# Kernel optimization log

Measured on AMD Instinct MI355X. Metric: run time of the kernel, lower is better.

Reference implementation:

```python
import jax, jax.numpy as jnp
import numpy as np

N_HEADS = 16
ROPE_THETA = 10000.0


def _rope_tables(seq_len, head_dim, dtype=jnp.float32):
    half = head_dim // 2
    inv_freq = 1.0 / (ROPE_THETA ** (jnp.arange(0, half, dtype=jnp.float32) / half))
    t = jnp.arange(seq_len, dtype=jnp.float32)
    freqs = jnp.outer(t, inv_freq)  # (S, half)
    return jnp.cos(freqs).astype(dtype), jnp.sin(freqs).astype(dtype)


def _apply_rope(x, cos, sin):
    # x: (B, H, S, hd); cos/sin: (S, hd//2)
    half = x.shape[-1] // 2
    x1, x2 = x[..., :half], x[..., half:]
    c = cos[None, None, :, :]
    s = sin[None, None, :, :]
    return jnp.concatenate([x1 * c - x2 * s, x1 * s + x2 * c], axis=-1)


def setup_inputs() -> dict:
    key = jax.random.key(0)
    k1, k2, k3 = jax.random.split(key, 3)
    B, S, D = 4, 2048, 2048
    hd = D // N_HEADS
    x = jax.random.normal(k1, (B, S, D), dtype=jnp.float32)
    cos, sin = _rope_tables(S, hd)
    w_qkv = jax.random.normal(k2, (D, 3 * D), dtype=jnp.float32) * (D ** -0.5)
    w_out = jax.random.normal(k3, (D, D), dtype=jnp.float32) * (D ** -0.5)
    return {"x": x, "cos": cos, "sin": sin, "w_qkv": w_qkv, "w_out": w_out}


def reference(x, cos, sin, w_qkv, w_out):
    B, S, D = x.shape
    H = N_HEADS
    hd = D // H
    qkv = x @ w_qkv  # (B, S, 3D)
    qkv = qkv.reshape(B, S, 3, H, hd).transpose(2, 0, 3, 1, 4)  # (3, B, H, S, hd)
    q, k, v = qkv[0], qkv[1], qkv[2]
    q = _apply_rope(q, cos, sin)
    k = _apply_rope(k, cos, sin)
    scale = 1.0 / jnp.sqrt(jnp.asarray(hd, dtype=x.dtype))
    scores = jnp.einsum('bhqd,bhkd->bhqk', q, k) * scale  # (B, H, S, S)
    causal = jnp.tril(jnp.ones((S, S), dtype=bool))
    scores = jnp.where(causal[None, None, :, :], scores, jnp.asarray(-1e30, dtype=scores.dtype))
    p = jax.nn.softmax(scores, axis=-1)
    out = jnp.einsum('bhqk,bhkd->bhqd', p, v)  # (B, H, S, hd)
    out = out.transpose(0, 2, 1, 3).reshape(B, S, D)
    return out @ w_out
```

## Files before the change

kernel.cpp:

```cpp
#include <hip/hip_runtime.h>
#include <stdint.h>

typedef __bf16  bf16x8  __attribute__((ext_vector_type(8)));
typedef float   floatx4 __attribute__((ext_vector_type(4)));

typedef __attribute__((address_space(1))) void gvoid_t;
typedef __attribute__((address_space(3))) void svoid_t;

__device__ __forceinline__ void gld16(ushort* lds, const ushort* g) {
  __builtin_amdgcn_global_load_lds((gvoid_t*)g, (svoid_t*)lds, 16, 0, 0);
}

__device__ __forceinline__ ushort f2bf(float f) {
  union { float f; unsigned u; } v; v.f = f;
  unsigned u = v.u;
  return (ushort)((u + 0x7fffu + ((u >> 16) & 1u)) >> 16);
}
__device__ __forceinline__ float bf2f(ushort h) {
  union { unsigned u; float f; } v; v.u = ((unsigned)h) << 16; return v.f;
}

__device__ __forceinline__ float qmax16(float v) {
  v = fmaxf(v, __shfl_xor(v, 1));
  v = fmaxf(v, __shfl_xor(v, 2));
  v = fmaxf(v, __shfl_xor(v, 4));
  v = fmaxf(v, __shfl_xor(v, 8));
  return v;
}
__device__ __forceinline__ float qsum16(float v) {
  v += __shfl_xor(v, 1);
  v += __shfl_xor(v, 2);
  v += __shfl_xor(v, 4);
  v += __shfl_xor(v, 8);
  return v;
}

__global__ __launch_bounds__(256) void cvt_f32_bf16(
    const float* __restrict__ in, ushort* __restrict__ out) {
  int i = blockIdx.x * 256 + threadIdx.x;
  float4 a = ((const float4*)in)[i];
  ushort4 o;
  o.x = f2bf(a.x); o.y = f2bf(a.y); o.z = f2bf(a.z); o.w = f2bf(a.w);
  ((ushort4*)out)[i] = o;
}

__global__ __launch_bounds__(256) void transpose_cvt(
    const float* __restrict__ in, ushort* __restrict__ out, int R, int C) {
  __shared__ ushort tile[64][65];
  const int r0 = blockIdx.y * 64, c0 = blockIdx.x * 64;
  const int t = threadIdx.x;
#pragma unroll
  for (int rep = 0; rep < 16; rep++) {
    int idx = rep * 256 + t;
    int r = idx >> 6, c = idx & 63;
    tile[r][c] = f2bf(in[(size_t)(r0 + r) * C + c0 + c]);
  }
  __syncthreads();
#pragma unroll
  for (int rep = 0; rep < 16; rep++) {
    int idx = rep * 256 + t;
    int r = idx >> 6, c = idx & 63;
    out[(size_t)(c0 + r) * R + r0 + c] = tile[c][r];
  }
}

template <int EPI>
__global__ __launch_bounds__(256) void gemm128(
    const ushort* __restrict__ A, const ushort* __restrict__ Bt,
    float* __restrict__ Cf,
    ushort* __restrict__ C0, ushort* __restrict__ C1, ushort* __restrict__ C2,
    int M, int N, int K) {
  __shared__ __align__(16) ushort As[128 * 64];
  __shared__ __align__(16) ushort Bs[128 * 64];
  const int t = threadIdx.x;
  const int lane = t & 63;
  const int w = t >> 6;
  const int l15 = lane & 15;
  const int quad = lane >> 4;
  const int m0 = blockIdx.y * 128;
  const int n0 = blockIdx.x * 128;
  const int wm = (w >> 1) * 64;
  const int wn = (w & 1) * 64;

  floatx4 acc[4][4];
  const floatx4 zero = {0.f, 0.f, 0.f, 0.f};
#pragma unroll
  for (int i = 0; i < 4; i++)
#pragma unroll
    for (int j = 0; j < 4; j++) acc[i][j] = zero;

  for (int kb = 0; kb < K; kb += 64) {
    __syncthreads();
#pragma unroll
    for (int it = 0; it < 4; it++) {
      int o = (w * 4 + it) * 64 + lane;
      int row = o >> 3;
      int c = (o & 7) ^ (row & 7);
      gld16(&As[(w * 4 + it) * 512], A + (size_t)(m0 + row) * K + kb + c * 8);
      gld16(&Bs[(w * 4 + it) * 512], Bt + (size_t)(n0 + row) * K + kb + c * 8);
    }
    __syncthreads();
#pragma unroll
    for (int kk = 0; kk < 2; kk++) {
      bf16x8 af[4], bf[4];
#pragma unroll
      for (int i = 0; i < 4; i++) {
        int row = wm + i * 16 + l15;
        int c = (kk * 4 + quad) ^ (row & 7);
        af[i] = *(const bf16x8*)&As[row * 64 + c * 8];
      }
#pragma unroll
      for (int j = 0; j < 4; j++) {
        int row = wn + j * 16 + l15;
        int c = (kk * 4 + quad) ^ (row & 7);
        bf[j] = *(const bf16x8*)&Bs[row * 64 + c * 8];
      }
#pragma unroll
      for (int i = 0; i < 4; i++)
#pragma unroll
        for (int j = 0; j < 4; j++)
          acc[i][j] = __builtin_amdgcn_mfma_f32_16x16x32_bf16(af[i], bf[j],
                                                              acc[i][j], 0, 0, 0);
    }
  }

  if (EPI == 0) {
#pragma unroll
    for (int i = 0; i < 4; i++)
#pragma unroll
      for (int j = 0; j < 4; j++)
#pragma unroll
        for (int r = 0; r < 4; r++) {
          int m = m0 + wm + i * 16 + quad * 4 + r;
          int n = n0 + wn + j * 16 + l15;
          Cf[(size_t)m * N + n] = acc[i][j][r];
        }
  } else {
    const int qkvsel = n0 >> 11;
    const int h = (n0 >> 7) & 15;
#pragma unroll
    for (int i = 0; i < 4; i++)
#pragma unroll
      for (int j = 0; j < 4; j++) {
        int d = wn + j * 16 + l15;
        if (qkvsel < 2) {
          ushort* dst = (qkvsel == 0) ? C0 : C1;
#pragma unroll
          for (int r = 0; r < 4; r++) {
            int m = m0 + wm + i * 16 + quad * 4 + r;
            int b = m >> 11, s = m & 2047;
            dst[((size_t)(b * 16 + h) * 2048 + s) * 128 + d] = f2bf(acc[i][j][r]);
          }
        } else {
          int m = m0 + wm + i * 16 + quad * 4;
          int b = m >> 11, s = m & 2047;
          ushort4 pk;
          pk.x = f2bf(acc[i][j][0]);
          pk.y = f2bf(acc[i][j][1]);
          pk.z = f2bf(acc[i][j][2]);
          pk.w = f2bf(acc[i][j][3]);
          *(ushort4*)&C2[((size_t)(b * 16 + h) * 128 + d) * 2048 + s] = pk;
        }
      }
  }
}

__global__ __launch_bounds__(256) void rope_kernel(
    ushort* __restrict__ Q, ushort* __restrict__ Kb,
    const float* __restrict__ cosT, const float* __restrict__ sinT) {
  unsigned gid = blockIdx.x * 256u + threadIdx.x;
  int d = gid & 63;
  int s = (gid >> 6) & 2047;
  int bh = (gid >> 17) & 63;
  ushort* buf = (gid >> 23) ? Kb : Q;
  size_t base = ((size_t)bh * 2048 + s) * 128;
  float x1 = bf2f(buf[base + d]);
  float x2 = bf2f(buf[base + d + 64]);
  float c = cosT[s * 64 + d];
  float sn = sinT[s * 64 + d];
  buf[base + d] = f2bf(x1 * c - x2 * sn);
  buf[base + d + 64] = f2bf(x1 * sn + x2 * c);
}

__global__ __launch_bounds__(256, 4) void attn_kernel(
    const ushort* __restrict__ Q, const ushort* __restrict__ Kb,
    const ushort* __restrict__ VT, ushort* __restrict__ O) {
  __shared__ __align__(16) ushort Ks[64 * 128];
  __shared__ __align__(16) ushort Vs[128 * 64];
  __shared__ __align__(16) ushort Ps[64 * 64];
  const int t = threadIdx.x, lane = t & 63, w = t >> 6;
  const int l15 = lane & 15, quad = lane >> 4;
  const int bid = blockIdx.x;
  const int tq = 31 - (bid >> 6);
  const int bh = bid & 63;
  const int q0 = tq * 64 + w * 16;
  const size_t hbase = (size_t)bh * 2048 * 128;
  const float NEGINF = -__builtin_inff();

  bf16x8 aq[4];
#pragma unroll
  for (int kb = 0; kb < 4; kb++)
    aq[kb] = *(const bf16x8*)&Q[hbase + (size_t)(q0 + l15) * 128 +
                                kb * 32 + quad * 8];

  float m2[4], lsum[4];
  floatx4 oacc[8];
  const floatx4 zero = {0.f, 0.f, 0.f, 0.f};
#pragma unroll
  for (int r = 0; r < 4; r++) { m2[r] = NEGINF; lsum[r] = 0.f; }
#pragma unroll
  for (int dj = 0; dj < 8; dj++) oacc[dj] = zero;

  const float sl2e = 0.08838834764831845f * 1.4426950408889634f;
  const int ntk = tq + 1;

  for (int tk = 0; tk < ntk; tk++) {
    __syncthreads();
#pragma unroll
    for (int it = 0; it < 4; it++) {
      int o = (w * 4 + it) * 64 + lane;
      {
        int row = o >> 4;
        int c = (o & 15) ^ (row & 15);
        gld16(&Ks[(w * 4 + it) * 512],
              Kb + hbase + (size_t)(tk * 64 + row) * 128 + c * 8);
      }
      {
        int row = o >> 3;
        int c = (o & 7) ^ (row & 7);
        gld16(&Vs[(w * 4 + it) * 512],
              VT + hbase + (size_t)row * 2048 + tk * 64 + c * 8);
      }
    }
    __syncthreads();

    floatx4 sacc[4];
#pragma unroll
    for (int j = 0; j < 4; j++) sacc[j] = zero;
#pragma unroll
    for (int kb = 0; kb < 4; kb++) {
#pragma unroll
      for (int j = 0; j < 4; j++) {
        int row = j * 16 + l15;
        int c = (kb * 4 + quad) ^ (row & 15);
        bf16x8 bk = *(const bf16x8*)&Ks[row * 128 + c * 8];
        sacc[j] = __builtin_amdgcn_mfma_f32_16x16x32_bf16(aq[kb], bk, sacc[j],
                                                          0, 0, 0);
      }
    }

    const bool need_mask = (tk == tq);
#pragma unroll
    for (int j = 0; j < 4; j++)
#pragma unroll
      for (int r = 0; r < 4; r++) {
        float v = sacc[j][r] * sl2e;
        if (need_mask) {
          int col = tk * 64 + j * 16 + l15;
          int row = q0 + quad * 4 + r;
          if (col > row) v = NEGINF;
        }
        sacc[j][r] = v;
      }
#pragma unroll
    for (int r = 0; r < 4; r++) {
      float mx = fmaxf(fmaxf(sacc[0][r], sacc[1][r]),
                       fmaxf(sacc[2][r], sacc[3][r]));
      mx = qmax16(mx);
      float mnew = fmaxf(m2[r], mx);
      float alpha = __builtin_exp2f(m2[r] - mnew);
      m2[r] = mnew;
      float rs = 0.f;
#pragma unroll
      for (int j = 0; j < 4; j++) {
        float p = __builtin_exp2f(sacc[j][r] - mnew);
        sacc[j][r] = p;
        rs += p;
      }
      rs = qsum16(rs);
      lsum[r] = lsum[r] * alpha + rs;
#pragma unroll
      for (int dj = 0; dj < 8; dj++) oacc[dj][r] *= alpha;
    }

#pragma unroll
    for (int j = 0; j < 4; j++)
#pragma unroll
      for (int r = 0; r < 4; r++) {
        int prow = w * 16 + quad * 4 + r;
        int col = j * 16 + l15;
        int scol = (((col >> 3) ^ (prow & 7)) << 3) | (col & 7);
        Ps[prow * 64 + scol] = f2bf(sacc[j][r]);
      }

    bf16x8 ap[2];
#pragma unroll
    for (int kk = 0; kk < 2; kk++) {
      int row = w * 16 + l15;
      int c = (kk * 4 + quad) ^ (row & 7);
      ap[kk] = *(const bf16x8*)&Ps[row * 64 + c * 8];
    }
#pragma unroll
    for (int kk = 0; kk < 2; kk++)
#pragma unroll
      for (int dj = 0; dj < 8; dj++) {
        int rowd = dj * 16 + l15;
        int c = (kk * 4 + quad) ^ (rowd & 7);
        bf16x8 bv = *(const bf16x8*)&Vs[rowd * 64 + c * 8];
        oacc[dj] = __builtin_amdgcn_mfma_f32_16x16x32_bf16(ap[kk], bv, oacc[dj],
                                                           0, 0, 0);
      }
  }

  const int b = bh >> 4, h = bh & 15;
  float rinv[4];
#pragma unroll
  for (int r = 0; r < 4; r++) rinv[r] = 1.0f / lsum[r];
#pragma unroll
  for (int dj = 0; dj < 8; dj++) {
    int d = dj * 16 + l15;
#pragma unroll
    for (int r = 0; r < 4; r++) {
      int q = q0 + quad * 4 + r;
      O[((size_t)(b * 2048 + q)) * 2048 + h * 128 + d] =
          f2bf(oacc[dj][r] * rinv[r]);
    }
  }
}

extern "C" void kernel_launch(void* const* d_in, const int* in_sizes, int n_in,
                              void* d_out, int out_size, void* d_ws, size_t ws_size,
                              hipStream_t stream) {
  const float* x    = (const float*)d_in[0];
  const float* cosT = (const float*)d_in[1];
  const float* sinT = (const float*)d_in[2];
  const float* wqkv = (const float*)d_in[3];
  const float* wout = (const float*)d_in[4];
  float* out = (float*)d_out;
  char* ws = (char*)d_ws;

  ushort* xbf   = (ushort*)d_out;
  ushort* wqkvT = (ushort*)(ws);
  ushort* Ob    = (ushort*)(ws);
  ushort* woutT = (ushort*)(ws + 33554432);
  ushort* Qb    = (ushort*)(ws + 41943040);
  ushort* Kbuf  = (ushort*)(ws + 75497472);
  ushort* VTb   = (ushort*)(ws + 109051904);

  cvt_f32_bf16<<<16384, 256, 0, stream>>>(x, xbf);
  transpose_cvt<<<dim3(96, 32), 256, 0, stream>>>(wqkv, wqkvT, 2048, 6144);
  transpose_cvt<<<dim3(32, 32), 256, 0, stream>>>(wout, woutT, 2048, 2048);
  gemm128<1><<<dim3(48, 64), 256, 0, stream>>>(xbf, wqkvT, nullptr,
                                               Qb, Kbuf, VTb, 8192, 6144, 2048);
  rope_kernel<<<65536, 256, 0, stream>>>(Qb, Kbuf, cosT, sinT);
  attn_kernel<<<2048, 256, 0, stream>>>(Qb, Kbuf, VTb, Ob);
  gemm128<0><<<dim3(16, 64), 256, 0, stream>>>(Ob, woutT, out,
                                               nullptr, nullptr, nullptr,
                                               8192, 2048, 2048);
}
```

Baseline: 730.0 us.

## Transpose attention MFMAs so each lane owns one query row

The QK^T and PV MFMA operand order is swapped, so the score and output accumulators are transposed and each lane holds a single query row. Softmax max and sum then reduce within the lane plus two cross-quad shuffles instead of 16-lane shuffle trees, and the per-row state collapses to scalars. The softmax scale and log2e factor are folded into Q during RoPE. P is written to LDS with packed bf16 stores, output is written with vectorized 4-element stores, and the rescale of the O accumulator is skipped when no row's max changed. Folding the scale into Q before bf16 rounding changes numerics slightly.

```diff
diff --git a/kernel.cpp b/kernel.cpp
--- a/kernel.cpp
+++ b/kernel.cpp
@@ -1,4 +1,5 @@
 #include <hip/hip_runtime.h>
+#include <hip/hip_bf16.h>
 #include <stdint.h>
 
 typedef __bf16  bf16x8  __attribute__((ext_vector_type(8)));
@@ -19,20 +20,9 @@
 __device__ __forceinline__ float bf2f(ushort h) {
   union { unsigned u; float f; } v; v.u = ((unsigned)h) << 16; return v.f;
 }
-
-__device__ __forceinline__ float qmax16(float v) {
-  v = fmaxf(v, __shfl_xor(v, 1));
-  v = fmaxf(v, __shfl_xor(v, 2));
-  v = fmaxf(v, __shfl_xor(v, 4));
-  v = fmaxf(v, __shfl_xor(v, 8));
-  return v;
-}
-__device__ __forceinline__ float qsum16(float v) {
-  v += __shfl_xor(v, 1);
-  v += __shfl_xor(v, 2);
-  v += __shfl_xor(v, 4);
-  v += __shfl_xor(v, 8);
-  return v;
+__device__ __forceinline__ unsigned pk2bf(float a, float b) {
+  __hip_bfloat162 h = __float22bfloat162_rn(make_float2(a, b));
+  union { __hip_bfloat162 h; unsigned u; } v; v.h = h; return v.u;
 }
 
 __global__ __launch_bounds__(256) void cvt_f32_bf16(
@@ -172,14 +162,17 @@
   int d = gid & 63;
   int s = (gid >> 6) & 2047;
   int bh = (gid >> 17) & 63;
-  ushort* buf = (gid >> 23) ? Kb : Q;
+  const bool isK = (gid >> 23) != 0;
+  ushort* buf = isK ? Kb : Q;
+  const float sc = isK ? 1.0f
+                       : 0.08838834764831845f * 1.4426950408889634f;
   size_t base = ((size_t)bh * 2048 + s) * 128;
   float x1 = bf2f(buf[base + d]);
   float x2 = bf2f(buf[base + d + 64]);
   float c = cosT[s * 64 + d];
   float sn = sinT[s * 64 + d];
-  buf[base + d] = f2bf(x1 * c - x2 * sn);
-  buf[base + d + 64] = f2bf(x1 * sn + x2 * c);
+  buf[base + d] = f2bf((x1 * c - x2 * sn) * sc);
+  buf[base + d + 64] = f2bf((x1 * sn + x2 * c) * sc);
 }
 
 __global__ __launch_bounds__(256, 4) void attn_kernel(
@@ -194,24 +187,21 @@
   const int tq = 31 - (bid >> 6);
   const int bh = bid & 63;
   const int q0 = tq * 64 + w * 16;
+  const int qrow = q0 + l15;
   const size_t hbase = (size_t)bh * 2048 * 128;
   const float NEGINF = -__builtin_inff();
 
   bf16x8 aq[4];
 #pragma unroll
   for (int kb = 0; kb < 4; kb++)
-    aq[kb] = *(const bf16x8*)&Q[hbase + (size_t)(q0 + l15) * 128 +
-                                kb * 32 + quad * 8];
-
-  float m2[4], lsum[4];
+    aq[kb] = *(const bf16x8*)&Q[hbase + (size_t)qrow * 128 + kb * 32 + quad * 8];
+
+  float m2 = NEGINF, lsum = 0.f;
   floatx4 oacc[8];
   const floatx4 zero = {0.f, 0.f, 0.f, 0.f};
 #pragma unroll
-  for (int r = 0; r < 4; r++) { m2[r] = NEGINF; lsum[r] = 0.f; }
-#pragma unroll
   for (int dj = 0; dj < 8; dj++) oacc[dj] = zero;
 
-  const float sl2e = 0.08838834764831845f * 1.4426950408889634f;
   const int ntk = tq + 1;
 
   for (int tk = 0; tk < ntk; tk++) {
@@ -243,62 +233,65 @@
       for (int j = 0; j < 4; j++) {
         int row = j * 16 + l15;
         int c = (kb * 4 + quad) ^ (row & 15);
-        bf16x8 bk = *(const bf16x8*)&Ks[row * 128 + c * 8];
-        sacc[j] = __builtin_amdgcn_mfma_f32_16x16x32_bf16(aq[kb], bk, sacc[j],
+        bf16x8 kf = *(const bf16x8*)&Ks[row * 128 + c * 8];
+        sacc[j] = __builtin_amdgcn_mfma_f32_16x16x32_bf16(kf, aq[kb], sacc[j],
                                                           0, 0, 0);
       }
     }
 
-    const bool need_mask = (tk == tq);
+    if (tk == tq) {
+#pragma unroll
+      for (int j = 0; j < 4; j++)
+#pragma unroll
+        for (int r = 0; r < 4; r++) {
+          int kcol = tk * 64 + j * 16 + quad * 4 + r;
+          if (kcol > qrow) sacc[j][r] = NEGINF;
+        }
+    }
+
+    float mx = sacc[0][0];
 #pragma unroll
     for (int j = 0; j < 4; j++)
 #pragma unroll
+      for (int r = 0; r < 4; r++) mx = fmaxf(mx, sacc[j][r]);
+    mx = fmaxf(mx, __shfl_xor(mx, 16));
+    mx = fmaxf(mx, __shfl_xor(mx, 32));
+    float mnew = fmaxf(m2, mx);
+    float alpha = __builtin_exp2f(m2 - mnew);
+    m2 = mnew;
+    float rs = 0.f;
+#pragma unroll
+    for (int j = 0; j < 4; j++)
+#pragma unroll
       for (int r = 0; r < 4; r++) {
-        float v = sacc[j][r] * sl2e;
-        if (need_mask) {
-          int col = tk * 64 + j * 16 + l15;
-          int row = q0 + quad * 4 + r;
-          if (col > row) v = NEGINF;
-        }
-        sacc[j][r] = v;
-      }
-#pragma unroll
-    for (int r = 0; r < 4; r++) {
-      float mx = fmaxf(fmaxf(sacc[0][r], sacc[1][r]),
-                       fmaxf(sacc[2][r], sacc[3][r]));
-      mx = qmax16(mx);
-      float mnew = fmaxf(m2[r], mx);
-      float alpha = __builtin_exp2f(m2[r] - mnew);
-      m2[r] = mnew;
-      float rs = 0.f;
-#pragma unroll
-      for (int j = 0; j < 4; j++) {
         float p = __builtin_exp2f(sacc[j][r] - mnew);
         sacc[j][r] = p;
         rs += p;
       }
-      rs = qsum16(rs);
-      lsum[r] = lsum[r] * alpha + rs;
-#pragma unroll
-      for (int dj = 0; dj < 8; dj++) oacc[dj][r] *= alpha;
-    }
-
-#pragma unroll
-    for (int j = 0; j < 4; j++)
-#pragma unroll
-      for (int r = 0; r < 4; r++) {
-        int prow = w * 16 + quad * 4 + r;
-        int col = j * 16 + l15;
-        int scol = (((col >> 3) ^ (prow & 7)) << 3) | (col & 7);
-        Ps[prow * 64 + scol] = f2bf(sacc[j][r]);
-      }
-
-    bf16x8 ap[2];
+    rs += __shfl_xor(rs, 16);
+    rs += __shfl_xor(rs, 32);
+    lsum = lsum * alpha + rs;
+    if (__any(alpha < 1.0f)) {
+#pragma unroll
+      for (int dj = 0; dj < 8; dj++) oacc[dj] *= alpha;
+    }
+
+#pragma unroll
+    for (int j = 0; j < 4; j++) {
+      unsigned lo = pk2bf(sacc[j][0], sacc[j][1]);
+      unsigned hi = pk2bf(sacc[j][2], sacc[j][3]);
+      int g = j * 2 + (quad >> 1);
+      int gp = g ^ (l15 & 7);
+      uint2 pv; pv.x = lo; pv.y = hi;
+      *(uint2*)&Ps[(w * 16 + l15) * 64 + gp * 8 + (quad & 1) * 4] = pv;
+    }
+
+    bf16x8 bp[2];
 #pragma unroll
     for (int kk = 0; kk < 2; kk++) {
-      int row = w * 16 + l15;
-      int c = (kk * 4 + quad) ^ (row & 7);
-      ap[kk] = *(const bf16x8*)&Ps[row * 64 + c * 8];
+      int g = kk * 4 + quad;
+      int gp = g ^ (l15 & 7);
+      bp[kk] = *(const bf16x8*)&Ps[(w * 16 + l15) * 64 + gp * 8];
     }
 #pragma unroll
     for (int kk = 0; kk < 2; kk++)
@@ -306,25 +299,23 @@
       for (int dj = 0; dj < 8; dj++) {
         int rowd = dj * 16 + l15;
         int c = (kk * 4 + quad) ^ (rowd & 7);
-        bf16x8 bv = *(const bf16x8*)&Vs[rowd * 64 + c * 8];
-        oacc[dj] = __builtin_amdgcn_mfma_f32_16x16x32_bf16(ap[kk], bv, oacc[dj],
+        bf16x8 av = *(const bf16x8*)&Vs[rowd * 64 + c * 8];
+        oacc[dj] = __builtin_amdgcn_mfma_f32_16x16x32_bf16(av, bp[kk], oacc[dj],
                                                            0, 0, 0);
       }
   }
 
   const int b = bh >> 4, h = bh & 15;
-  float rinv[4];
-#pragma unroll
-  for (int r = 0; r < 4; r++) rinv[r] = 1.0f / lsum[r];
+  const float rl = 1.0f / lsum;
+  const size_t obase = ((size_t)(b * 2048 + qrow)) * 2048 + h * 128;
 #pragma unroll
   for (int dj = 0; dj < 8; dj++) {
-    int d = dj * 16 + l15;
-#pragma unroll
-    for (int r = 0; r < 4; r++) {
-      int q = q0 + quad * 4 + r;
-      O[((size_t)(b * 2048 + q)) * 2048 + h * 128 + d] =
-          f2bf(oacc[dj][r] * rinv[r]);
-    }
+    ushort4 pk;
+    pk.x = f2bf(oacc[dj][0] * rl);
+    pk.y = f2bf(oacc[dj][1] * rl);
+    pk.z = f2bf(oacc[dj][2] * rl);
+    pk.w = f2bf(oacc[dj][3] * rl);
+    *(ushort4*)&O[obase + dj * 16 + quad * 4] = pk;
   }
 }
 
```

Result: faster. 637.0 us (-12.7%).
